# Performance work log

Hardware: AMD Instinct MI355X
Metric: run time of the kernel (lower is better)

Reference implementation:

```python
import jax, jax.numpy as jnp
import numpy as np
import itertools
from jax import lax

KERNEL_SIZE = 3
ITERATION = 12
PAD = KERNEL_SIZE // 2
# offsets in the exact order torch code generates them: product([0,1,-1], repeat=2)
OFFSETS = list(itertools.product([*range(KERNEL_SIZE // 2 + 1), *range(-(KERNEL_SIZE // 2), 0)], repeat=2))


def setup_inputs() -> dict:
    key = jax.random.key(0)
    k1, k2, k3, k4 = jax.random.split(key, 4)
    B, C, H, W = 4, 32, 480, 640
    kernel_x = jax.random.normal(k1, (B, C, H, W), jnp.float32)
    x = jax.random.normal(k2, (B, 1, H, W), jnp.float32)
    W_aff = jax.random.normal(k3, (KERNEL_SIZE ** 2 - 1, C, 3, 3), jnp.float32) * 0.05
    b_aff = jax.random.normal(k4, (KERNEL_SIZE ** 2 - 1,), jnp.float32) * 0.05
    return {"kernel_x": kernel_x, "x": x, "W_aff": W_aff, "b_aff": b_aff}


def _gen_kernel(aff):
    # aff: [B, k^2-1, H, W] -> normalized affinity kernel [B, k^2, H, W]
    abs_sum = jnp.sum(jnp.abs(aff), axis=1, keepdims=True)
    a = aff / abs_sum
    s = jnp.sum(a, axis=1, keepdims=True)
    return jnp.concatenate([1.0 - s, a], axis=1)


def _im2col(x):
    # x: [B, 1, H, W] -> shifted copies [B, k^2, H, W] with zero padding,
    # out[:, k, p] = x[:, 0, p - offset_k]
    B, _, H, W = x.shape
    xp = jnp.pad(x[:, 0], ((0, 0), (PAD, PAD), (PAD, PAD)))
    cols = [xp[:, PAD - oi:PAD - oi + H, PAD - oj:PAD - oj + W] for (oi, oj) in OFFSETS]
    return jnp.stack(cols, axis=1)


def reference(kernel_x, x, W_aff, b_aff):
    # affinity_net: 3x3 conv, 32 -> 8 channels, SAME padding
    aff = lax.conv_general_dilated(
        kernel_x, W_aff, window_strides=(1, 1), padding="SAME",
        dimension_numbers=("NCHW", "OIHW", "NCHW"),
    ) + b_aff[None, :, None, None]
    kernel = _gen_kernel(aff)  # [B, 9, H, W]
    for _ in range(ITERATION):
        x = jnp.sum(_im2col(x) * kernel, axis=1, keepdims=True)
    return x
```

## Files before the change

kernel.cpp:

```cpp
#include <hip/hip_runtime.h>
#include <hip/hip_fp16.h>

#define BB 4
#define CC 32
#define HH 480
#define WW 640
#define HWv (HH*WW)

union H8 { __half h[8]; float4 f4; };

__global__ __launch_bounds__(128) void conv_gen(const float* __restrict__ kx,
                                                const float* __restrict__ Wf,
                                                const float* __restrict__ bf,
                                                __half* __restrict__ K)
{
    int tid = blockIdx.x * 128 + threadIdx.x;
    const int XT = WW / 8;
    int x8 = tid % XT;
    int t2 = tid / XT;
    int y  = t2 % HH;
    int b  = t2 / HH;
    if (b >= BB) return;
    int x0 = x8 * 8;

    float acc[8][8];
#pragma unroll
    for (int o = 0; o < 8; ++o) {
        float bv = bf[o];
#pragma unroll
        for (int p = 0; p < 8; ++p) acc[o][p] = bv;
    }

    const float* kxb = kx + (size_t)b * CC * HWv + (size_t)y * WW + x0;
    const bool xm = (x0 > 0);
    const bool xp = (x0 + 8 < WW);

    for (int c = 0; c < CC; ++c) {
        const float* pl = kxb + (size_t)c * HWv;
#pragma unroll
        for (int r = 0; r < 3; ++r) {
            const int dy = r - 1;
            const bool rowok = (y + dy >= 0) && (y + dy < HH);
            const float* rp = pl + dy * WW;
            float row[10];
            if (rowok) {
                float4 v0 = *reinterpret_cast<const float4*>(rp);
                float4 v1 = *reinterpret_cast<const float4*>(rp + 4);
                row[0] = xm ? rp[-1] : 0.f;
                row[1] = v0.x; row[2] = v0.y; row[3] = v0.z; row[4] = v0.w;
                row[5] = v1.x; row[6] = v1.y; row[7] = v1.z; row[8] = v1.w;
                row[9] = xp ? rp[8] : 0.f;
            } else {
#pragma unroll
                for (int q = 0; q < 10; ++q) row[q] = 0.f;
            }
#pragma unroll
            for (int o = 0; o < 8; ++o) {
#pragma unroll
                for (int t = 0; t < 3; ++t) {
                    float wv = Wf[((o * CC + c) * 3 + r) * 3 + t];
#pragma unroll
                    for (int p = 0; p < 8; ++p) acc[o][p] += wv * row[p + t];
                }
            }
        }
    }

    float k0[8];
#pragma unroll
    for (int p = 0; p < 8; ++p) {
        float asum = 0.f;
#pragma unroll
        for (int o = 0; o < 8; ++o) asum += fabsf(acc[o][p]);
        float rinv = 1.0f / asum;
        float s = 0.f;
#pragma unroll
        for (int o = 0; o < 8; ++o) { acc[o][p] *= rinv; s += acc[o][p]; }
        k0[p] = 1.0f - s;
    }

    size_t base = (size_t)b * 9 * HWv + (size_t)y * WW + x0;
    {
        H8 u;
#pragma unroll
        for (int p = 0; p < 8; ++p) u.h[p] = __float2half(k0[p]);
        *reinterpret_cast<float4*>(K + base) = u.f4;
    }
#pragma unroll
    for (int o = 0; o < 8; ++o) {
        H8 u;
#pragma unroll
        for (int p = 0; p < 8; ++p) u.h[p] = __float2half(acc[o][p]);
        *reinterpret_cast<float4*>(K + base + (size_t)(o + 1) * HWv) = u.f4;
    }
}

__device__ __forceinline__ void load_row6(const float* r, bool rowok, bool xm,
                                          bool xpl, float o[6])
{
    if (rowok) {
        float4 v = *reinterpret_cast<const float4*>(r);
        o[0] = xm ? r[-1] : 0.f;
        o[1] = v.x; o[2] = v.y; o[3] = v.z; o[4] = v.w;
        o[5] = xpl ? r[4] : 0.f;
    } else {
#pragma unroll
        for (int q = 0; q < 6; ++q) o[q] = 0.f;
    }
}

union H4 { short4 s; __half h[4]; };

__global__ __launch_bounds__(256) void prop(const float* __restrict__ xin,
                                            const __half* __restrict__ K,
                                            float* __restrict__ xout)
{
    int tid = blockIdx.x * 256 + threadIdx.x;
    const int XT = WW / 4;
    int x4 = tid % XT;
    int t2 = tid / XT;
    int y  = t2 % HH;
    int b  = t2 / HH;
    if (b >= BB) return;
    int x0 = x4 * 4;

    const bool xm  = (x0 > 0);
    const bool xpl = (x0 + 4 < WW);

    const float* xb = xin + (size_t)b * HWv + (size_t)y * WW + x0;
    float rm[6], r0[6], rp[6];
    load_row6(xb - WW, y > 0,      xm, xpl, rm);
    load_row6(xb,      true,       xm, xpl, r0);
    load_row6(xb + WW, y < HH - 1, xm, xpl, rp);

    const __half* Kb = K + (size_t)b * 9 * HWv + (size_t)y * WW + x0;
    float kv[9][4];
#pragma unroll
    for (int k = 0; k < 9; ++k) {
        H4 u;
        u.s = *reinterpret_cast<const short4*>(Kb + (size_t)k * HWv);
#pragma unroll
        for (int p = 0; p < 4; ++p) kv[k][p] = __half2float(u.h[p]);
    }

    float out[4];
#pragma unroll
    for (int p = 0; p < 4; ++p) {
        out[p] = kv[0][p] * r0[p + 1]
               + kv[1][p] * r0[p]
               + kv[2][p] * r0[p + 2]
               + kv[3][p] * rm[p + 1]
               + kv[4][p] * rm[p]
               + kv[5][p] * rm[p + 2]
               + kv[6][p] * rp[p + 1]
               + kv[7][p] * rp[p]
               + kv[8][p] * rp[p + 2];
    }

    *reinterpret_cast<float4*>(xout + (size_t)b * HWv + (size_t)y * WW + x0) =
        make_float4(out[0], out[1], out[2], out[3]);
}

extern "C" void kernel_launch(void* const* d_in, const int* in_sizes, int n_in,
                              void* d_out, int out_size, void* d_ws, size_t ws_size,
                              hipStream_t stream) {
    const float* kx   = (const float*)d_in[0];
    const float* x_in = (const float*)d_in[1];
    const float* Wf   = (const float*)d_in[2];
    const float* bf   = (const float*)d_in[3];
    float* out  = (float*)d_out;

    __half* Kbuf = (__half*)d_ws;
    float*  xbuf = (float*)((char*)d_ws +
                            (size_t)9 * BB * HWv * sizeof(__half));

    const int cthreads = BB * HH * (WW / 8);
    conv_gen<<<cthreads / 128, 128, 0, stream>>>(kx, Wf, bf, Kbuf);

    const int pthreads = BB * HH * (WW / 4);
    const int pblocks  = pthreads / 256;

    const float* src = x_in;
    for (int it = 0; it < 12; ++it) {
        float* dst = (it % 2 == 0) ? xbuf : out;
        prop<<<pblocks, 256, 0, stream>>>(src, Kbuf, dst);
        src = dst;
    }
}
```

Before: 170.7 us.

## Rewrite affinity conv as fp16 MFMA implicit GEMM with LDS tiling

Replaces the scalar FP32 3x3 conv (32->8 channels) with a tiled kernel. It stages an 8x64 input tile of all channels, converted to fp16, into swizzled shared memory, then computes each of the 9 taps with 16x16x32 f16 MFMA instructions. Normalization uses cross-lane shuffles, and the results are transposed through LDS for coalesced half stores. This moves the conv's FMA work onto matrix cores and cuts redundant global loads. In exchange the conv inputs and weights lose precision to fp16, and half the MFMA output columns are padding.

```diff
diff --git a/kernel.cpp b/kernel.cpp
--- a/kernel.cpp
+++ b/kernel.cpp
@@ -7,91 +7,136 @@
 #define WW 640
 #define HWv (HH*WW)
 
-union H8 { __half h[8]; float4 f4; };
-
-__global__ __launch_bounds__(128) void conv_gen(const float* __restrict__ kx,
-                                                const float* __restrict__ Wf,
-                                                const float* __restrict__ bf,
-                                                __half* __restrict__ K)
+typedef _Float16 f16x8 __attribute__((ext_vector_type(8)));
+typedef _Float16 f16x2 __attribute__((ext_vector_type(2)));
+typedef float f32x4 __attribute__((ext_vector_type(4)));
+
+#define CR 8
+#define CCOL 64
+#define SR 10
+#define SC 72
+
+__global__ __launch_bounds__(256, 2) void conv_mfma(const float* __restrict__ kx,
+                                                    const float* __restrict__ Wf,
+                                                    const float* __restrict__ bf,
+                                                    _Float16* __restrict__ K)
 {
-    int tid = blockIdx.x * 128 + threadIdx.x;
-    const int XT = WW / 8;
-    int x8 = tid % XT;
-    int t2 = tid / XT;
-    int y  = t2 % HH;
-    int b  = t2 / HH;
-    if (b >= BB) return;
-    int x0 = x8 * 8;
-
-    float acc[8][8];
-#pragma unroll
-    for (int o = 0; o < 8; ++o) {
-        float bv = bf[o];
-#pragma unroll
-        for (int p = 0; p < 8; ++p) acc[o][p] = bv;
-    }
-
-    const float* kxb = kx + (size_t)b * CC * HWv + (size_t)y * WW + x0;
-    const bool xm = (x0 > 0);
-    const bool xp = (x0 + 8 < WW);
-
-    for (int c = 0; c < CC; ++c) {
-        const float* pl = kxb + (size_t)c * HWv;
-#pragma unroll
-        for (int r = 0; r < 3; ++r) {
-            const int dy = r - 1;
-            const bool rowok = (y + dy >= 0) && (y + dy < HH);
-            const float* rp = pl + dy * WW;
-            float row[10];
-            if (rowok) {
-                float4 v0 = *reinterpret_cast<const float4*>(rp);
-                float4 v1 = *reinterpret_cast<const float4*>(rp + 4);
-                row[0] = xm ? rp[-1] : 0.f;
-                row[1] = v0.x; row[2] = v0.y; row[3] = v0.z; row[4] = v0.w;
-                row[5] = v1.x; row[6] = v1.y; row[7] = v1.z; row[8] = v1.w;
-                row[9] = xp ? rp[8] : 0.f;
-            } else {
-#pragma unroll
-                for (int q = 0; q < 10; ++q) row[q] = 0.f;
+    __shared__ _Float16 smem[SR * SC * CC];
+
+    const int t    = threadIdx.x;
+    const int lane = t & 63;
+    const int wv   = t >> 6;
+    const int n    = lane & 15;
+    const int ks   = lane >> 4;
+
+    int blk = blockIdx.x;
+    const int xt = blk % (WW / CCOL); blk /= (WW / CCOL);
+    const int yt = blk % (HH / CR);
+    const int b  = blk / (HH / CR);
+    const int y0 = yt * CR;
+    const int x0 = xt * CCOL;
+
+    f16x8 btap[9];
+#pragma unroll
+    for (int tp = 0; tp < 9; ++tp) {
+#pragma unroll
+        for (int j = 0; j < 8; ++j) {
+            float w = (n < 8) ? Wf[(n * CC + (ks * 8 + j)) * 9 + tp] : 0.f;
+            btap[tp][j] = (_Float16)w;
+        }
+    }
+    const float bfv = (n < 8) ? bf[n] : 0.f;
+
+    const float* kxb = kx + (size_t)b * CC * HWv;
+#pragma unroll
+    for (int s = 0; s < 12; ++s) {
+        int u = s * 256 + t;
+        if (u < SR * SC * 4) {
+            int xcol = u % SC;
+            int yc   = u / SC;
+            int yy   = yc >> 2;
+            int co   = yc & 3;
+            int gx = x0 - 4 + xcol;
+            int gy = y0 - 1 + yy;
+            bool ok = (gx >= 0) && (gx < WW) && (gy >= 0) && (gy < HH);
+            const float* sp = kxb + (size_t)(co * 8) * HWv
+                            + (size_t)(ok ? gy : 0) * WW + (ok ? gx : 0);
+            f16x8 h;
+#pragma unroll
+            for (int j = 0; j < 8; ++j) {
+                float v = ok ? sp[(size_t)j * HWv] : 0.f;
+                h[j] = (_Float16)v;
             }
-#pragma unroll
-            for (int o = 0; o < 8; ++o) {
-#pragma unroll
-                for (int t = 0; t < 3; ++t) {
-                    float wv = Wf[((o * CC + c) * 3 + r) * 3 + t];
-#pragma unroll
-                    for (int p = 0; p < 8; ++p) acc[o][p] += wv * row[p + t];
-                }
+            int ba = ((yy * SC + xcol) * CC + co * 8) * 2;
+            ba ^= ((xcol >> 1) & 7) << 4;
+            *reinterpret_cast<f16x8*>(reinterpret_cast<char*>(smem) + ba) = h;
+        }
+    }
+    __syncthreads();
+
+    f32x4 acc[8];
+#pragma unroll
+    for (int g = 0; g < 8; ++g) acc[g] = f32x4{bfv, bfv, bfv, bfv};
+
+#pragma unroll
+    for (int g = 0; g < 8; ++g) {
+        int rl = wv * 2 + (g & 1);
+        int xg = g >> 1;
+#pragma unroll
+        for (int ty = 0; ty < 3; ++ty) {
+#pragma unroll
+            for (int tx = 0; tx < 3; ++tx) {
+                int xcol = xg * 16 + n + tx + 3;
+                int ba = (((rl + ty) * SC + xcol) * CC + ks * 8) * 2;
+                ba ^= ((xcol >> 1) & 7) << 4;
+                f16x8 a = *reinterpret_cast<const f16x8*>(
+                              reinterpret_cast<const char*>(smem) + ba);
+                acc[g] = __builtin_amdgcn_mfma_f32_16x16x32_f16(
+                             a, btap[ty * 3 + tx], acc[g], 0, 0, 0);
             }
         }
     }
-
-    float k0[8];
-#pragma unroll
-    for (int p = 0; p < 8; ++p) {
-        float asum = 0.f;
-#pragma unroll
-        for (int o = 0; o < 8; ++o) asum += fabsf(acc[o][p]);
-        float rinv = 1.0f / asum;
-        float s = 0.f;
-#pragma unroll
-        for (int o = 0; o < 8; ++o) { acc[o][p] *= rinv; s += acc[o][p]; }
-        k0[p] = 1.0f - s;
-    }
-
-    size_t base = (size_t)b * 9 * HWv + (size_t)y * WW + x0;
-    {
-        H8 u;
-#pragma unroll
-        for (int p = 0; p < 8; ++p) u.h[p] = __float2half(k0[p]);
-        *reinterpret_cast<float4*>(K + base) = u.f4;
-    }
-#pragma unroll
-    for (int o = 0; o < 8; ++o) {
-        H8 u;
-#pragma unroll
-        for (int p = 0; p < 8; ++p) u.h[p] = __float2half(acc[o][p]);
-        *reinterpret_cast<float4*>(K + base + (size_t)(o + 1) * HWv) = u.f4;
+    __syncthreads();
+
+    _Float16* outa = smem;
+#pragma unroll
+    for (int g = 0; g < 8; ++g) {
+        int rl = wv * 2 + (g & 1);
+        int xg = g >> 1;
+        float aff[4], sa[4], ss[4];
+#pragma unroll
+        for (int r = 0; r < 4; ++r) {
+            aff[r] = (n < 8) ? acc[g][r] : 0.f;
+            sa[r]  = fabsf(aff[r]);
+            ss[r]  = aff[r];
+        }
+#pragma unroll
+        for (int wdt = 1; wdt <= 4; wdt <<= 1) {
+#pragma unroll
+            for (int r = 0; r < 4; ++r) {
+                sa[r] += __shfl_xor(sa[r], wdt);
+                ss[r] += __shfl_xor(ss[r], wdt);
+            }
+        }
+#pragma unroll
+        for (int r = 0; r < 4; ++r) {
+            float rinv = 1.0f / sa[r];
+            float av   = aff[r] * rinv;
+            float k0   = 1.0f - ss[r] * rinv;
+            int px = rl * 64 + xg * 16 + ks * 4 + r;
+            if (n < 8)  outa[px * 10 + n + 1] = (_Float16)av;
+            if (n == 0) outa[px * 10 + 0]     = (_Float16)k0;
+        }
+    }
+    __syncthreads();
+
+    const int px0 = 2 * t;
+    _Float16* Kb = K + (size_t)b * 9 * HWv
+                 + (size_t)(y0 + (px0 >> 6)) * WW + x0 + (px0 & 63);
+#pragma unroll
+    for (int p = 0; p < 9; ++p) {
+        f16x2 v2 = { outa[px0 * 10 + p], outa[(px0 + 1) * 10 + p] };
+        *reinterpret_cast<f16x2*>(Kb + (size_t)p * HWv) = v2;
     }
 }
 
@@ -170,12 +215,12 @@
     const float* bf   = (const float*)d_in[3];
     float* out  = (float*)d_out;
 
-    __half* Kbuf = (__half*)d_ws;
-    float*  xbuf = (float*)((char*)d_ws +
-                            (size_t)9 * BB * HWv * sizeof(__half));
-
-    const int cthreads = BB * HH * (WW / 8);
-    conv_gen<<<cthreads / 128, 128, 0, stream>>>(kx, Wf, bf, Kbuf);
+    _Float16* Kbuf = (_Float16*)d_ws;
+    float*    xbuf = (float*)((char*)d_ws +
+                              (size_t)9 * BB * HWv * sizeof(_Float16));
+
+    const int cblocks = BB * (HH / CR) * (WW / CCOL);
+    conv_mfma<<<cblocks, 256, 0, stream>>>(kx, Wf, bf, Kbuf);
 
     const int pthreads = BB * HH * (WW / 4);
     const int pblocks  = pthreads / 256;
@@ -183,7 +228,7 @@
     const float* src = x_in;
     for (int it = 0; it < 12; ++it) {
         float* dst = (it % 2 == 0) ? xbuf : out;
-        prop<<<pblocks, 256, 0, stream>>>(src, Kbuf, dst);
+        prop<<<pblocks, 256, 0, stream>>>(src, (const __half*)Kbuf, dst);
         src = dst;
     }
 }
```

Measured after the change: 280.6 us. 1.64x slower.

## Fuse two propagation iterations per launch using shared-memory tiles with halo recompute

Applied to the files above, without the earlier changes.

Replaces the single-step propagation kernel with one that performs two iterations per launch. Each block stages a 16x64 tile of x plus a two-pixel halo in LDS and computes the intermediate step, including a one-pixel halo ring that is recomputed from reloaded affinity values. It then applies the second step from LDS, halving the number of launches and the global reads and writes of x and K. In exchange it adds redundant halo computation, scalar uncoalesced K loads for halo pixels, and two block barriers per launch.

```diff
diff --git a/kernel.cpp b/kernel.cpp
--- a/kernel.cpp
+++ b/kernel.cpp
@@ -8,6 +8,7 @@
 #define HWv (HH*WW)
 
 union H8 { __half h[8]; float4 f4; };
+union H4 { short4 s; __half h[4]; };
 
 __global__ __launch_bounds__(128) void conv_gen(const float* __restrict__ kx,
                                                 const float* __restrict__ Wf,
@@ -95,70 +96,119 @@
     }
 }
 
-__device__ __forceinline__ void load_row6(const float* r, bool rowok, bool xm,
-                                          bool xpl, float o[6])
+#define P2R 16
+#define P2C 64
+#define XSTR 73
+
+__global__ __launch_bounds__(256) void prop2(const float* __restrict__ xin,
+                                             const __half* __restrict__ Kk,
+                                             float* __restrict__ xout)
 {
-    if (rowok) {
-        float4 v = *reinterpret_cast<const float4*>(r);
-        o[0] = xm ? r[-1] : 0.f;
-        o[1] = v.x; o[2] = v.y; o[3] = v.z; o[4] = v.w;
-        o[5] = xpl ? r[4] : 0.f;
-    } else {
-#pragma unroll
-        for (int q = 0; q < 6; ++q) o[q] = 0.f;
-    }
-}
-
-union H4 { short4 s; __half h[4]; };
-
-__global__ __launch_bounds__(256) void prop(const float* __restrict__ xin,
-                                            const __half* __restrict__ K,
-                                            float* __restrict__ xout)
-{
-    int tid = blockIdx.x * 256 + threadIdx.x;
-    const int XT = WW / 4;
-    int x4 = tid % XT;
-    int t2 = tid / XT;
-    int y  = t2 % HH;
-    int b  = t2 / HH;
-    if (b >= BB) return;
-    int x0 = x4 * 4;
-
-    const bool xm  = (x0 > 0);
-    const bool xpl = (x0 + 4 < WW);
-
-    const float* xb = xin + (size_t)b * HWv + (size_t)y * WW + x0;
-    float rm[6], r0[6], rp[6];
-    load_row6(xb - WW, y > 0,      xm, xpl, rm);
-    load_row6(xb,      true,       xm, xpl, r0);
-    load_row6(xb + WW, y < HH - 1, xm, xpl, rp);
-
-    const __half* Kb = K + (size_t)b * 9 * HWv + (size_t)y * WW + x0;
+    __shared__ float x0s[20 * XSTR];
+    __shared__ float x1s[18 * XSTR];
+
+    const int t  = threadIdx.x;
+    const int tx = t & 15;
+    const int ty = t >> 4;
+
+    int blk = blockIdx.x;
+    const int xt = blk % (WW / P2C); blk /= (WW / P2C);
+    const int yt = blk % (HH / P2R);
+    const int b  = blk / (HH / P2R);
+    const int y0  = yt * P2R;
+    const int xg0 = xt * P2C;
+
+    const float*  xb = xin + (size_t)b * HWv;
+    const __half* Kb = Kk  + (size_t)b * 9 * HWv;
+
+#pragma unroll
+    for (int pass = 0; pass < 6; ++pass) {
+        int u = pass * 256 + t;
+        if (u < 20 * 68) {
+            int r = u / 68, c = u - (u / 68) * 68;
+            int gy = y0 - 2 + r, gx = xg0 - 2 + c;
+            bool ok = (gy >= 0 && gy < HH && gx >= 0 && gx < WW);
+            x0s[r * XSTR + c] = ok ? xb[(size_t)gy * WW + gx] : 0.f;
+        }
+    }
+
     float kv[9][4];
-#pragma unroll
-    for (int k = 0; k < 9; ++k) {
-        H4 u;
-        u.s = *reinterpret_cast<const short4*>(Kb + (size_t)k * HWv);
-#pragma unroll
-        for (int p = 0; p < 4; ++p) kv[k][p] = __half2float(u.h[p]);
-    }
-
-    float out[4];
+    {
+        const __half* kp = Kb + (size_t)(y0 + ty) * WW + xg0 + 4 * tx;
+#pragma unroll
+        for (int k = 0; k < 9; ++k) {
+            H4 u;
+            u.s = *reinterpret_cast<const short4*>(kp + (size_t)k * HWv);
+#pragma unroll
+            for (int p = 0; p < 4; ++p) kv[k][p] = __half2float(u.h[p]);
+        }
+    }
+    __syncthreads();
+
+#define X0(r, c) x0s[((r) + 2) * XSTR + ((c) + 2)]
+#define X1(r, c) x1s[((r) + 1) * XSTR + ((c) + 1)]
+
 #pragma unroll
     for (int p = 0; p < 4; ++p) {
-        out[p] = kv[0][p] * r0[p + 1]
-               + kv[1][p] * r0[p]
-               + kv[2][p] * r0[p + 2]
-               + kv[3][p] * rm[p + 1]
-               + kv[4][p] * rm[p]
-               + kv[5][p] * rm[p + 2]
-               + kv[6][p] * rp[p + 1]
-               + kv[7][p] * rp[p]
-               + kv[8][p] * rp[p + 2];
-    }
-
-    *reinterpret_cast<float4*>(xout + (size_t)b * HWv + (size_t)y * WW + x0) =
-        make_float4(out[0], out[1], out[2], out[3]);
+        int c = 4 * tx + p, r = ty;
+        float v = kv[0][p] * X0(r, c)
+                + kv[1][p] * X0(r, c - 1)
+                + kv[2][p] * X0(r, c + 1)
+                + kv[3][p] * X0(r - 1, c)
+                + kv[4][p] * X0(r - 1, c - 1)
+                + kv[5][p] * X0(r - 1, c + 1)
+                + kv[6][p] * X0(r + 1, c)
+                + kv[7][p] * X0(r + 1, c - 1)
+                + kv[8][p] * X0(r + 1, c + 1);
+        X1(r, c) = v;
+    }
+
+    if (t < 164) {
+        int hr, hc;
+        if      (t <  66) { hr = -1;      hc = t - 1;   }
+        else if (t < 132) { hr = 16;      hc = t - 67;  }
+        else if (t < 148) { hr = t - 132; hc = -1;      }
+        else              { hr = t - 148; hc = 64;      }
+        int gy = y0 + hr, gx = xg0 + hc;
+        bool in = (gy >= 0 && gy < HH && gx >= 0 && gx < WW);
+        int gyc = gy < 0 ? 0 : (gy > HH - 1 ? HH - 1 : gy);
+        int gxc = gx < 0 ? 0 : (gx > WW - 1 ? WW - 1 : gx);
+        const __half* kp = Kb + (size_t)gyc * WW + gxc;
+        float hk[9];
+#pragma unroll
+        for (int k = 0; k < 9; ++k) hk[k] = __half2float(kp[(size_t)k * HWv]);
+        float v = hk[0] * X0(hr, hc)
+                + hk[1] * X0(hr, hc - 1)
+                + hk[2] * X0(hr, hc + 1)
+                + hk[3] * X0(hr - 1, hc)
+                + hk[4] * X0(hr - 1, hc - 1)
+                + hk[5] * X0(hr - 1, hc + 1)
+                + hk[6] * X0(hr + 1, hc)
+                + hk[7] * X0(hr + 1, hc - 1)
+                + hk[8] * X0(hr + 1, hc + 1);
+        X1(hr, hc) = in ? v : 0.f;
+    }
+    __syncthreads();
+
+    float o4[4];
+#pragma unroll
+    for (int p = 0; p < 4; ++p) {
+        int c = 4 * tx + p, r = ty;
+        o4[p] = kv[0][p] * X1(r, c)
+              + kv[1][p] * X1(r, c - 1)
+              + kv[2][p] * X1(r, c + 1)
+              + kv[3][p] * X1(r - 1, c)
+              + kv[4][p] * X1(r - 1, c - 1)
+              + kv[5][p] * X1(r - 1, c + 1)
+              + kv[6][p] * X1(r + 1, c)
+              + kv[7][p] * X1(r + 1, c - 1)
+              + kv[8][p] * X1(r + 1, c + 1);
+    }
+    *reinterpret_cast<float4*>(xout + (size_t)b * HWv
+                               + (size_t)(y0 + ty) * WW + xg0 + 4 * tx) =
+        make_float4(o4[0], o4[1], o4[2], o4[3]);
+#undef X0
+#undef X1
 }
 
 extern "C" void kernel_launch(void* const* d_in, const int* in_sizes, int n_in,
@@ -177,13 +227,11 @@
     const int cthreads = BB * HH * (WW / 8);
     conv_gen<<<cthreads / 128, 128, 0, stream>>>(kx, Wf, bf, Kbuf);
 
-    const int pthreads = BB * HH * (WW / 4);
-    const int pblocks  = pthreads / 256;
-
+    const int pblocks = BB * (HH / P2R) * (WW / P2C);
     const float* src = x_in;
-    for (int it = 0; it < 12; ++it) {
-        float* dst = (it % 2 == 0) ? xbuf : out;
-        prop<<<pblocks, 256, 0, stream>>>(src, Kbuf, dst);
+    for (int l = 0; l < 6; ++l) {
+        float* dst = (l % 2 == 0) ? xbuf : out;
+        prop2<<<pblocks, 256, 0, stream>>>(src, Kbuf, dst);
         src = dst;
     }
 }
```

Result: no change. 169.5 us (-0.8%).
